# Optimization experiments

Measured on AMD Instinct MI355X. Metric: run time of the kernel, lower is better.

The kernel has to match this reference:

```python
import jax, jax.numpy as jnp
import numpy as np
import math

LMAX = 2
NUM_RBF = 32
CUTOFF = 5.0
MUL_EDGE = 4          # mul_per_l
N_NODES = 50000
N_EDGES = 800000
NODE_MULS = [64, 32, 16]   # multiplicities of 0e,1o,2e in node_irreps
MSG_MULS = [64, 32, 16]    # multiplicities of 0e,1o,2e in msg_irreps
NODE_DIM = sum(m * (2 * l + 1) for l, m in enumerate(NODE_MULS))  # 240
# parity-conserving CG paths (l1 from node, l2 from edge, l3 to msg)
PATHS = [(0,0,0),(1,1,0),(2,2,0),(0,1,1),(1,0,1),(1,2,1),(2,1,1),(0,2,2),(2,0,2),(1,1,2),(2,2,2)]
TP_SIZES = [NODE_MULS[l1]*MUL_EDGE*MSG_MULS[l3] for (l1,l2,l3) in PATHS]
FAN_IN = {l3: sum(NODE_MULS[p1]*MUL_EDGE for (p1,p2,p3) in PATHS if p3 == l3) for l3 in range(LMAX+1)}


def _su2_cg(j1, m1, j2, m2, j3, m3):
    # Racah formula for SU(2) Clebsch-Gordan coefficients (integer l)
    if m3 != m1 + m2:
        return 0.0
    f = lambda n: math.factorial(int(n))
    vmin = int(max(-j1 + j2 + m3, -j1 + m1, 0))
    vmax = int(min(j2 + j3 + m1, j3 - j1 + j2, j3 + m3))
    C = math.sqrt((2*j3+1) * f(j3+j1-j2) * f(j3-j1+j2) * f(j1+j2-j3) * f(j3+m3) * f(j3-m3)
                  / (f(j1+j2+j3+1) * f(j1-m1) * f(j1+m1) * f(j2-m2) * f(j2+m2)))
    S = 0.0
    for v in range(vmin, vmax+1):
        S += (-1.0)**(v + j2 + m2) * f(j2+j3+m1-v) * f(j1-m1+v) / (
            f(v) * f(j3-j1+j2-v) * f(j3+m3-v) * f(v+j1-j2-m3))
    return C * S


def _real_to_complex(l):
    # change of basis real spherical harmonics -> complex, with phase making 3j real
    q = np.zeros((2*l+1, 2*l+1), dtype=np.complex128)
    for m in range(-l, 0):
        q[l+m, l+abs(m)] = 1/math.sqrt(2)
        q[l+m, l-abs(m)] = -1j/math.sqrt(2)
    q[l, l] = 1.0
    for m in range(1, l+1):
        q[l+m, l+abs(m)] = (-1)**m / math.sqrt(2)
        q[l+m, l-abs(m)] = 1j*(-1)**m / math.sqrt(2)
    return (-1j)**l * q


def _wigner_3j(l1, l2, l3):
    C = np.zeros((2*l1+1, 2*l2+1, 2*l3+1))
    for m1 in range(-l1, l1+1):
        for m2 in range(-l2, l2+1):
            for m3 in range(-l3, l3+1):
                C[l1+m1, l2+m2, l3+m3] = _su2_cg(l1, m1, l2, m2, l3, m3)
    Q1, Q2, Q3 = _real_to_complex(l1), _real_to_complex(l2), _real_to_complex(l3)
    Cc = np.einsum('ij,kl,mn,ikn->jlm', Q1, Q2, np.conj(Q3).T, C.astype(np.complex128))
    Cr = np.real(Cc)
    if np.linalg.norm(Cr) < 1e-8:
        Cr = np.imag(Cc)
    return (Cr / np.linalg.norm(Cr)).astype(np.float32)

W3J = {p: jnp.asarray(_wigner_3j(*p)) for p in PATHS}


def setup_inputs() -> dict:
    key = jax.random.key(0)
    ks = jax.random.split(key, 8)
    node_feat = jax.random.normal(ks[0], (N_NODES, NODE_DIM), jnp.float32)
    edge_index = jax.random.randint(ks[1], (2, N_EDGES), 0, N_NODES)
    edge_vec = jax.random.normal(ks[2], (N_EDGES, 3), jnp.float32) * 1.5
    mask = jax.random.uniform(ks[3], (N_EDGES,), jnp.float32)
    mlp_w1 = jax.random.normal(ks[4], (LMAX+1, NUM_RBF, 32), jnp.float32) / math.sqrt(NUM_RBF)
    mlp_b1 = jnp.zeros((LMAX+1, 32), jnp.float32)
    mlp_w2 = jax.random.normal(ks[5], (LMAX+1, 32, MUL_EDGE), jnp.float32) / math.sqrt(32.0)
    mlp_b2 = jnp.zeros((LMAX+1, MUL_EDGE), jnp.float32)
    tp_w = jax.random.normal(ks[6], (sum(TP_SIZES),), jnp.float32)
    return {"node_feat": node_feat, "edge_index": edge_index, "edge_vec": edge_vec,
            "mask": mask, "mlp_w1": mlp_w1, "mlp_b1": mlp_b1,
            "mlp_w2": mlp_w2, "mlp_b2": mlp_b2, "tp_w": tp_w}


def reference(node_feat, edge_index, edge_vec, mask, mlp_w1, mlp_b1, mlp_w2, mlp_b2, tp_w):
    src = edge_index[0]
    r = jnp.maximum(jnp.linalg.norm(edge_vec, axis=-1, keepdims=True), 1e-12)   # [E,1]
    r_hat = edge_vec / r
    x, y, z = r_hat[:, 0], r_hat[:, 1], r_hat[:, 2]
    # --- RBFEmb (smooth cosine cutoff + gaussians in exp(-r) space), then the
    # extra rbounds factor applied again in _edge_features (faithful to source)
    rbounds = 0.5 * (jnp.cos(r * jnp.pi / CUTOFF) + 1.0)                         # [E,1]
    means = jnp.linspace(math.exp(-CUTOFF), 1.0, NUM_RBF).astype(edge_vec.dtype)
    beta = (2.0 / NUM_RBF * (1.0 - math.exp(-CUTOFF))) ** (-2)
    rbf = rbounds * (r < CUTOFF).astype(edge_vec.dtype) * jnp.exp(-beta * jnp.square(jnp.exp(-r) - means))
    rbf = rbounds * rbf                                                          # [E,NUM_RBF]
    # --- real spherical harmonics, e3nn 'component' normalization, l = 0,1,2
    s3, s5, s15 = math.sqrt(3.0), math.sqrt(5.0), math.sqrt(15.0)
    Y = [jnp.ones_like(x)[:, None],
         s3 * r_hat,
         jnp.stack([s15 * x * z, s15 * x * y, s5 * (y * y - 0.5 * (x * x + z * z)),
                    s15 * y * z, 0.5 * s15 * (z * z - x * x)], axis=-1)]
    # --- per-l radial MLP weights, outer product with Y_l -> edge irrep blocks
    edge_blocks = []
    for l in range(LMAX + 1):
        h = jax.nn.silu(rbf @ mlp_w1[l] + mlp_b1[l])
        w_l = h @ mlp_w2[l] + mlp_b2[l]                                          # [E,MUL_EDGE]
        edge_blocks.append(w_l[:, :, None] * Y[l][:, None, :])                   # [E,MUL_EDGE,2l+1]
    # --- gather node features per edge and split into irrep blocks
    f_i = node_feat[src]                                                         # [E,NODE_DIM]
    node_blocks, off = [], 0
    for l, mul in enumerate(NODE_MULS):
        d = mul * (2 * l + 1)
        node_blocks.append(f_i[:, off:off + d].reshape(-1, mul, 2 * l + 1))
        off += d
    # --- fully-connected CG tensor product (per-path small contractions)
    terms = {l3: [] for l3 in range(LMAX + 1)}
    woff = 0
    for (l1, l2, l3), sz in zip(PATHS, TP_SIZES):
        W = tp_w[woff:woff + sz].reshape(NODE_MULS[l1], MUL_EDGE, MSG_MULS[l3])
        woff += sz
        alpha = 1.0 / math.sqrt(FAN_IN[l3])
        terms[l3].append(alpha * jnp.einsum('eui,evj,uvw,ijk->ewk',
                                            node_blocks[l1], edge_blocks[l2], W,
                                            W3J[(l1, l2, l3)], optimize='optimal'))
    E = edge_vec.shape[0]
    msg_e = jnp.concatenate([sum(terms[l3]).reshape(E, -1) for l3 in range(LMAX + 1)], axis=-1)
    return msg_e * mask[:, None]
```

## Files before the change

### kernel.cpp

```cpp
#include <hip/hip_runtime.h>
#include <math.h>

#define TE 32
#define NODE_DIM 240
#define NPAD 248

typedef _Float16 f16;
typedef f16 f16x2 __attribute__((ext_vector_type(2)));
typedef f16 f16x4 __attribute__((ext_vector_type(4)));
typedef f16 f16x8 __attribute__((ext_vector_type(8)));
typedef float f32x4 __attribute__((ext_vector_type(4)));


struct cplx { double re, im; };
__device__ inline cplx cmul(cplx a, cplx b) {
    return { a.re*b.re - a.im*b.im, a.re*b.im + a.im*b.re };
}

__device__ double dfact(int n) { double r = 1.0; for (int i = 2; i <= n; ++i) r *= i; return r; }

__device__ double su2_cg(int j1, int m1, int j2, int m2, int j3, int m3) {
    if (m3 != m1 + m2) return 0.0;
    int vmin = max(max(-j1 + j2 + m3, -j1 + m1), 0);
    int vmax = min(min(j2 + j3 + m1, j3 - j1 + j2), j3 + m3);
    double C = sqrt((2.0*j3 + 1.0) * dfact(j3 + j1 - j2) * dfact(j3 - j1 + j2) * dfact(j1 + j2 - j3)
                    * dfact(j3 + m3) * dfact(j3 - m3)
                    / (dfact(j1 + j2 + j3 + 1) * dfact(j1 - m1) * dfact(j1 + m1)
                       * dfact(j2 - m2) * dfact(j2 + m2)));
    double S = 0.0;
    for (int v = vmin; v <= vmax; ++v) {
        double sgn = ((v + j2 + m2) & 1) ? -1.0 : 1.0;
        S += sgn * dfact(j2 + j3 + m1 - v) * dfact(j1 - m1 + v)
             / (dfact(v) * dfact(j3 - j1 + j2 - v) * dfact(j3 + m3 - v) * dfact(v + j1 - j2 - m3));
    }
    return C * S;
}

__device__ cplx rtc(int l, int a, int b) {
    double re = 0.0, im = 0.0;
    const double inv_s2 = 0.70710678118654752440;
    int m = a - l;
    if (m < 0) {
        if (b == l - m)      re = inv_s2;
        else if (b == l + m) im = -inv_s2;
    } else if (m == 0) {
        if (b == l) re = 1.0;
    } else {
        double s = (m & 1) ? -1.0 : 1.0;
        if (b == l + m)      re = s * inv_s2;
        else if (b == l - m) im = s * inv_s2;
    }
    if (l == 1) { double t = re; re = im; im = -t; }
    else if (l == 2) { re = -re; im = -im; }
    return { re, im };
}

__global__ void w3j_init(float* __restrict__ out) {
    __shared__ double sRe[363], sIm[363];
    __shared__ double sNorm[11];
    __shared__ int    sUse[11];
    const int L1A[11] = {0,1,2,0,1,1,2,0,2,1,2};
    const int L2A[11] = {0,1,2,1,0,2,1,2,0,1,2};
    const int L3A[11] = {0,0,0,1,1,1,1,2,2,2,2};
    const int OFF[12] = {0,1,10,35,44,53,98,143,168,193,238,363};
    int t = threadIdx.x;
    if (t < 363) {
        int p = 0;
        while (p < 10 && t >= OFF[p+1]) ++p;
        int rel = t - OFF[p];
        int a1 = L1A[p], a2 = L2A[p], a3 = L3A[p];
        int n1 = 2*a1 + 1, n2 = 2*a2 + 1, n3 = 2*a3 + 1;
        int jj = rel / (n2*n3), ll = (rel / n3) % n2, mm = rel % n3;
        double cr = 0.0, ci = 0.0;
        for (int i = 0; i < n1; ++i)
            for (int k = 0; k < n2; ++k)
                for (int n = 0; n < n3; ++n) {
                    double c = su2_cg(a1, i - a1, a2, k - a2, a3, n - a3);
                    if (c == 0.0) continue;
                    cplx q1 = rtc(a1, i, jj);
                    cplx q2 = rtc(a2, k, ll);
                    cplx q3 = rtc(a3, n, mm); q3.im = -q3.im;
                    cplx pr = cmul(cmul(q1, q2), q3);
                    cr += pr.re * c; ci += pr.im * c;
                }
        sRe[t] = cr; sIm[t] = ci;
    }
    __syncthreads();
    if (t < 11) {
        double nr = 0.0, ni = 0.0;
        for (int e = OFF[t]; e < OFF[t+1]; ++e) { nr += sRe[e]*sRe[e]; ni += sIm[e]*sIm[e]; }
        int use_im = (sqrt(nr) < 1e-8) ? 1 : 0;
        sUse[t] = use_im;
        sNorm[t] = sqrt(use_im ? ni : nr);
    }
    __syncthreads();
    if (t < 363) {
        int p = 0;
        while (p < 10 && t >= OFF[p+1]) ++p;
        out[t] = (float)((sUse[p] ? sIm[t] : sRe[t]) / sNorm[p]);
    }
}

__global__ void w_prep(const float* __restrict__ tp_w, f16* __restrict__ wpre) {
    const int WOFF[11] = {0,16384,24576,28672,36864,40960,45056,47104,51200,52224,54272};
    const int UA[11]   = {64,32,16,64,32,32,16,64,16,32,16};
    const int NA[11]   = {64,64,64,32,32,32,32,16,16,16,16};
    const int L3A[11]  = {0,0,0,1,1,1,1,2,2,2,2};
    const float alph[3] = { 1.0f/sqrtf(448.0f), 1.0f/24.0f, 1.0f/sqrtf(512.0f) };
    int tid = threadIdx.x;
    for (int p = 0; p < 11; ++p) {
        int U = UA[p], N = NA[p], woff = WOFF[p];
        int NT = N/16;
        int size = U*4*N;
        float alpha = alph[L3A[p]];
        for (int j = tid; j < size; j += 256) {
            int f = j >> 9, r = j & 511;
            int lane = r >> 3, jj = r & 7;
            int ks = f / NT, nt = f - ks*NT;
            int k = ks*32 + (lane>>4)*8 + jj;
            int n = nt*16 + (lane&15);
            wpre[woff + j] = (f16)(tp_w[woff + k*N + n] * alpha);
        }
    }
}

template<int l1, int l2, int l3>
__device__ __forceinline__ void path_mfma(
    int tid, int woff, int cgoff,
    const f16* __restrict__ wpre,
    const f16* sN16, const float (*sY)[8], const float* sW3,
    const f16x2 (*sWlPk)[6],
    f32x4 (&acc)[3])
{
    constexpr int U  = (l1 == 0) ? 64 : (l1 == 1) ? 32 : 16;
    constexpr int N  = (l3 == 0) ? 64 : (l3 == 1) ? 32 : 16;
    constexpr int NI = 2*l1 + 1, NJ = 2*l2 + 1, NK = 2*l3 + 1;
    constexpr int M  = NK * TE;
    constexpr int NODE_OFF = (l1 == 0) ? 0 : (l1 == 1) ? 64 : 160;
    constexpr int KS = U / 8;
    constexpr int NT = N / 16;
    constexpr int NTASKS = (M/16) * NT;

    const int wv = tid >> 6, lane = tid & 63;
    const int ln = tid & 15, qt = (tid & 63) >> 4;

    #pragma unroll
    for (int t = 0; t < 3; ++t) {
        int task = t*4 + wv;
        if (task < NTASKS) {
            int mt = task / NT, nt = task - mt*NT;
            int row = mt*16 + ln;
            int e = row & 31, kk = row >> 5;
            float cyr[NI];
            #pragma unroll
            for (int i = 0; i < NI; ++i) {
                float c = 0.f;
                #pragma unroll
                for (int j = 0; j < NJ; ++j) {
                    float yj = (l2 == 0) ? 1.f : ((l2 == 1) ? sY[e][j] : sY[e][3 + j]);
                    c += sW3[cgoff + (i*NJ + j)*NK + kk] * yj;
                }
                cyr[i] = c;
            }
            f16x2 wl0 = sWlPk[e][l2*2 + 0];
            f16x2 wl1 = sWlPk[e][l2*2 + 1];
            const f16* nbase = sN16 + e*NPAD + NODE_OFF;
            const f16* wbase = wpre + woff + (size_t)nt*512 + lane*8;
            #pragma unroll
            for (int ks = 0; ks < KS; ++ks) {
                f16x8 wf = *(const f16x8*)(wbase + (size_t)ks*NT*512);
                int u0 = ks*8 + qt*2;
                float b0 = 0.f, b1 = 0.f;
                #pragma unroll
                for (int i = 0; i < NI; ++i) {
                    b0 += (float)nbase[u0*NI + i]      * cyr[i];
                    b1 += (float)nbase[u0*NI + NI + i] * cyr[i];
                }
                f16 b0h = (f16)b0, b1h = (f16)b1;
                f16x2 bb0 = {b0h, b0h}, bb1 = {b1h, b1h};
                f16x2 a01 = bb0*wl0, a23 = bb0*wl1, a45 = bb1*wl0, a67 = bb1*wl1;
                f16x8 af = {a01[0],a01[1],a23[0],a23[1],a45[0],a45[1],a67[0],a67[1]};
                acc[t] = __builtin_amdgcn_mfma_f32_16x16x32_f16(af, wf, acc[t], 0, 0, 0);
            }
        }
    }
}

template<int NK, int NT, int NTASKS, int OFF>
__device__ __forceinline__ void store_group(int tid, const f32x4 (&acc)[3], f16* sAcc16)
{
    int wv = tid >> 6;
    int ln = tid & 15, qt = (tid & 63) >> 4;
    #pragma unroll
    for (int t = 0; t < 3; ++t) {
        int task = t*4 + wv;
        if (task < NTASKS) {
            int mt = task / NT, nt = task % NT;
            int kk = mt >> 1;
            int e0 = (mt & 1) * 16;
            #pragma unroll
            for (int r = 0; r < 4; ++r) {
                int e = e0 + qt*4 + r;
                sAcc16[e*240 + OFF + (nt*16 + ln)*NK + kk] = (f16)acc[t][r];
            }
        }
    }
}

__global__ __launch_bounds__(256, 4)
void edge_main(const float* __restrict__ node_feat,
               const int*   __restrict__ edge_src,
               const float* __restrict__ edge_vec,
               const float* __restrict__ maskp,
               const float* __restrict__ mlp_w1, const float* __restrict__ mlp_b1,
               const float* __restrict__ mlp_w2, const float* __restrict__ mlp_b2,
               const f16*   __restrict__ wpre,
               const float* __restrict__ w3j,
               float* __restrict__ out)
{
    __shared__ __align__(16) f16 sN16[TE*NPAD];
    __shared__ __align__(16) f16 sAcc16[TE*240];
    __shared__ float sW3[364];
    __shared__ float sY[TE][8];
    __shared__ f16x2 sWlPk[TE][6];

    float* sRbf  = (float*)sAcc16;
    float* sH    = sRbf + TE*32;
    float* sWl   = sH   + TE*32;
    float* sR    = sWl  + TE*12;
    float* sRb2  = sR   + TE;
    float* sMask = sRb2 + TE;
    int*   sSrc  = (int*)(sMask + TE);

    int tid = threadIdx.x;
    long eg0 = (long)blockIdx.x * TE;

    if (tid < TE) {
        long eg = eg0 + tid;
        float vx = edge_vec[eg*3 + 0], vy = edge_vec[eg*3 + 1], vz = edge_vec[eg*3 + 2];
        float rn = sqrtf(vx*vx + vy*vy + vz*vz);
        float r  = fmaxf(rn, 1e-12f);
        float inv = 1.0f / r;
        float x = vx*inv, y = vy*inv, z = vz*inv;
        sR[tid] = r;
        float rb = 0.5f * (cosf(r * 3.14159265358979323846f / 5.0f) + 1.0f);
        sRb2[tid] = (r < 5.0f) ? rb*rb : 0.0f;
        sMask[tid] = maskp[eg];
        sSrc[tid]  = edge_src[eg];
        const float s3 = sqrtf(3.0f), s5 = sqrtf(5.0f), s15 = sqrtf(15.0f);
        sY[tid][0] = s3*x; sY[tid][1] = s3*y; sY[tid][2] = s3*z;
        sY[tid][3] = s15*x*z;
        sY[tid][4] = s15*x*y;
        sY[tid][5] = s5*(y*y - 0.5f*(x*x + z*z));
        sY[tid][6] = s15*y*z;
        sY[tid][7] = 0.5f*s15*(z*z - x*x);
    }
    for (int t = tid; t < 363; t += 256) sW3[t] = w3j[t];
    __syncthreads();

    {
        float em5  = expf(-5.0f);
        float step = (1.0f - em5) / 31.0f;
        float beta = 256.0f / ((1.0f - em5) * (1.0f - em5));
        for (int idx = tid; idx < TE*32; idx += 256) {
            int e = idx >> 5, j = idx & 31;
            float mean = em5 + step * j;
            float d = expf(-sR[e]) - mean;
            sRbf[e*32 + j] = sRb2[e] * expf(-beta * d * d);
        }
    }
    for (int idx = tid; idx < TE*60; idx += 256) {
        int e = idx / 60, q = idx - e*60;
        f32x4 v = *(const f32x4*)(node_feat + (long)sSrc[e]*NODE_DIM + q*4);
        f16x4 h = {(f16)v.x, (f16)v.y, (f16)v.z, (f16)v.w};
        *(f16x4*)&sN16[e*NPAD + q*4] = h;
    }
    __syncthreads();

    for (int l = 0; l < 3; ++l) {
        for (int idx = tid; idx < TE*32; idx += 256) {
            int e = idx >> 5, j = idx & 31;
            float zacc = mlp_b1[l*32 + j];
            #pragma unroll 8
            for (int rr = 0; rr < 32; ++rr) zacc += sRbf[e*32 + rr] * mlp_w1[(l*32 + rr)*32 + j];
            sH[e*32 + j] = zacc / (1.0f + expf(-zacc));
        }
        __syncthreads();
        for (int idx = tid; idx < TE*4; idx += 256) {
            int e = idx >> 2, v = idx & 3;
            float zacc = mlp_b2[l*4 + v];
            #pragma unroll 8
            for (int j = 0; j < 32; ++j) zacc += sH[e*32 + j] * mlp_w2[(l*32 + j)*4 + v];
            sWl[e*12 + l*4 + v] = zacc;
        }
        __syncthreads();
    }
    for (int idx = tid; idx < TE*6; idx += 256) {
        int e = idx / 6, h = idx - e*6;
        int l = h >> 1, vh = h & 1;
        float m = sMask[e];
        f16x2 p = {(f16)(sWl[e*12 + l*4 + vh*2] * m), (f16)(sWl[e*12 + l*4 + vh*2 + 1] * m)};
        sWlPk[e][h] = p;
    }
    __syncthreads();

    f32x4 acc[3];

    #pragma unroll
    for (int t = 0; t < 3; ++t) acc[t] = {0.f, 0.f, 0.f, 0.f};
    path_mfma<0,0,0>(tid,     0,   0, wpre, sN16, sY, sW3, sWlPk, acc);
    path_mfma<1,1,0>(tid, 16384,   1, wpre, sN16, sY, sW3, sWlPk, acc);
    path_mfma<2,2,0>(tid, 24576,  10, wpre, sN16, sY, sW3, sWlPk, acc);
    store_group<1, 4, 8, 0>(tid, acc, sAcc16);

    #pragma unroll
    for (int t = 0; t < 3; ++t) acc[t] = {0.f, 0.f, 0.f, 0.f};
    path_mfma<0,1,1>(tid, 28672,  35, wpre, sN16, sY, sW3, sWlPk, acc);
    path_mfma<1,0,1>(tid, 36864,  44, wpre, sN16, sY, sW3, sWlPk, acc);
    path_mfma<1,2,1>(tid, 40960,  53, wpre, sN16, sY, sW3, sWlPk, acc);
    path_mfma<2,1,1>(tid, 45056,  98, wpre, sN16, sY, sW3, sWlPk, acc);
    store_group<3, 2, 12, 64>(tid, acc, sAcc16);

    #pragma unroll
    for (int t = 0; t < 3; ++t) acc[t] = {0.f, 0.f, 0.f, 0.f};
    path_mfma<0,2,2>(tid, 47104, 143, wpre, sN16, sY, sW3, sWlPk, acc);
    path_mfma<2,0,2>(tid, 51200, 168, wpre, sN16, sY, sW3, sWlPk, acc);
    path_mfma<1,1,2>(tid, 52224, 193, wpre, sN16, sY, sW3, sWlPk, acc);
    path_mfma<2,2,2>(tid, 54272, 238, wpre, sN16, sY, sW3, sWlPk, acc);
    store_group<5, 1, 10, 160>(tid, acc, sAcc16);

    __syncthreads();

    for (int idx = tid; idx < TE*30; idx += 256) {
        int e = idx / 30, q = idx - e*30;
        f16x8 v = *(const f16x8*)&sAcc16[e*240 + q*8];
        f32x4 lo = {(float)v[0], (float)v[1], (float)v[2], (float)v[3]};
        f32x4 hi = {(float)v[4], (float)v[5], (float)v[6], (float)v[7]};
        float* dst = out + (eg0 + e)*NODE_DIM + q*8;
        __builtin_nontemporal_store(lo, (f32x4*)dst);
        __builtin_nontemporal_store(hi, (f32x4*)(dst + 4));
    }
}

extern "C" void kernel_launch(void* const* d_in, const int* in_sizes, int n_in,
                              void* d_out, int out_size, void* d_ws, size_t ws_size,
                              hipStream_t stream)
{
    const float* node_feat = (const float*)d_in[0];
    const int*   edge_idx  = (const int*)  d_in[1];
    const float* edge_vec  = (const float*)d_in[2];
    const float* maskp     = (const float*)d_in[3];
    const float* mlp_w1    = (const float*)d_in[4];
    const float* mlp_b1    = (const float*)d_in[5];
    const float* mlp_w2    = (const float*)d_in[6];
    const float* mlp_b2    = (const float*)d_in[7];
    const float* tp_w      = (const float*)d_in[8];
    float* out  = (float*)d_out;
    float* w3j  = (float*)d_ws;
    f16*   wpre = (f16*)((char*)d_ws + 2048);

    int E = in_sizes[3];
    const int* edge_src = edge_idx;

    hipLaunchKernelGGL(w3j_init, dim3(1), dim3(512), 0, stream, w3j);
    hipLaunchKernelGGL(w_prep,   dim3(1), dim3(256), 0, stream, tp_w, wpre);
    hipLaunchKernelGGL(edge_main, dim3(E / TE), dim3(256), 0, stream,
                       node_feat, edge_src, edge_vec, maskp,
                       mlp_w1, mlp_b1, mlp_w2, mlp_b2, wpre, w3j, out);
}
```

Before: 1.173 ms.

## Pad node irrep blocks in LDS and use packed fdot2 for node-CG contraction

Node features are stored in shared memory with each l=1 and l=2 component group padded to 4 and 8 halfs, so one lane can fetch a multiplicity's components with a single 16-byte LDS load. The per-task CG-times-Y coefficients are precomputed once and packed to f16, and the node contraction uses packed fdot2 instead of scalar converts and FMAs. The loop order is also inverted so each weight fragment loaded from global memory is reused across all of a wave's M-tasks. In exchange, shared-memory use grows, the buffer must be zero-filled, the scatter into LDS for l>0 becomes scalar, and the coefficients lose precision by being rounded to f16.

```diff
diff --git a/kernel.cpp b/kernel.cpp
--- a/kernel.cpp
+++ b/kernel.cpp
@@ -3,13 +3,28 @@
 
 #define TE 32
 #define NODE_DIM 240
-#define NPAD 248
+#define ESTR 328
 
 typedef _Float16 f16;
 typedef f16 f16x2 __attribute__((ext_vector_type(2)));
 typedef f16 f16x4 __attribute__((ext_vector_type(4)));
 typedef f16 f16x8 __attribute__((ext_vector_type(8)));
 typedef float f32x4 __attribute__((ext_vector_type(4)));
+
+__device__ __forceinline__ float fdot2(f16x2 a, f16x2 b, float c) {
+#if __has_builtin(__builtin_amdgcn_fdot2)
+    return __builtin_amdgcn_fdot2(a, b, c, false);
+#else
+    return (float)a[0]*(float)b[0] + (float)a[1]*(float)b[1] + c;
+#endif
+}
+__device__ __forceinline__ f16x2 cvtpk(float a, float b) {
+#if __has_builtin(__builtin_amdgcn_cvt_pkrtz)
+    return __builtin_bit_cast(f16x2, __builtin_amdgcn_cvt_pkrtz(a, b));
+#else
+    f16x2 r = {(f16)a, (f16)b}; return r;
+#endif
+}
 
 
 struct cplx { double re, im; };
@@ -124,6 +139,12 @@
     }
 }
 
+__device__ __forceinline__ int node_slot(int ch) {
+    if (ch < 64) return ch;
+    if (ch < 160) { int t = ch - 64;  return 64  + (t/3)*4 + (t - (t/3)*3); }
+    { int t = ch - 160; return 192 + (t/5)*8 + (t - (t/5)*5); }
+}
+
 template<int l1, int l2, int l3>
 __device__ __forceinline__ void path_mfma(
     int tid, int woff, int cgoff,
@@ -136,21 +157,26 @@
     constexpr int N  = (l3 == 0) ? 64 : (l3 == 1) ? 32 : 16;
     constexpr int NI = 2*l1 + 1, NJ = 2*l2 + 1, NK = 2*l3 + 1;
     constexpr int M  = NK * TE;
-    constexpr int NODE_OFF = (l1 == 0) ? 0 : (l1 == 1) ? 64 : 160;
+    constexpr int SEC = (l1 == 0) ? 0 : (l1 == 1) ? 64 : 192;
     constexpr int KS = U / 8;
     constexpr int NT = N / 16;
     constexpr int NTASKS = (M/16) * NT;
+    constexpr int NW = (NTASKS + 3) / 4;
 
     const int wv = tid >> 6, lane = tid & 63;
     const int ln = tid & 15, qt = (tid & 63) >> 4;
-
-    #pragma unroll
-    for (int t = 0; t < 3; ++t) {
+    const int ntw = wv % NT;
+
+    const f16* nbT[NW];
+    f16x2 cyP[NW][3];
+    f16x2 wl0T[NW], wl1T[NW];
+    #pragma unroll
+    for (int t = 0; t < NW; ++t) {
         int task = t*4 + wv;
         if (task < NTASKS) {
-            int mt = task / NT, nt = task - mt*NT;
-            int row = mt*16 + ln;
-            int e = row & 31, kk = row >> 5;
+            int mt = task / NT;
+            int kk = mt >> 1;
+            int e  = (mt & 1)*16 + ln;
             float cyr[NI];
             #pragma unroll
             for (int i = 0; i < NI; ++i) {
@@ -162,23 +188,56 @@
                 }
                 cyr[i] = c;
             }
-            f16x2 wl0 = sWlPk[e][l2*2 + 0];
-            f16x2 wl1 = sWlPk[e][l2*2 + 1];
-            const f16* nbase = sN16 + e*NPAD + NODE_OFF;
-            const f16* wbase = wpre + woff + (size_t)nt*512 + lane*8;
-            #pragma unroll
-            for (int ks = 0; ks < KS; ++ks) {
-                f16x8 wf = *(const f16x8*)(wbase + (size_t)ks*NT*512);
-                int u0 = ks*8 + qt*2;
-                float b0 = 0.f, b1 = 0.f;
-                #pragma unroll
-                for (int i = 0; i < NI; ++i) {
-                    b0 += (float)nbase[u0*NI + i]      * cyr[i];
-                    b1 += (float)nbase[u0*NI + NI + i] * cyr[i];
+            if constexpr (NI == 1) {
+                cyP[t][0] = cvtpk(cyr[0], cyr[0]);
+            } else if constexpr (NI == 3) {
+                cyP[t][0] = cvtpk(cyr[0], cyr[1]);
+                cyP[t][1] = cvtpk(cyr[2], 0.f);
+            } else {
+                cyP[t][0] = cvtpk(cyr[0], cyr[1]);
+                cyP[t][1] = cvtpk(cyr[2], cyr[3]);
+                cyP[t][2] = cvtpk(cyr[4], 0.f);
+            }
+            wl0T[t] = sWlPk[e][l2*2 + 0];
+            wl1T[t] = sWlPk[e][l2*2 + 1];
+            nbT[t]  = sN16 + e*ESTR + SEC;
+        }
+    }
+
+    const f16* wbase = wpre + woff + (size_t)ntw*512 + lane*8;
+    #pragma unroll
+    for (int ks = 0; ks < KS; ++ks) {
+        f16x8 wf = *(const f16x8*)(wbase + (size_t)ks*NT*512);
+        const int u0 = ks*8 + qt*2;
+        #pragma unroll
+        for (int t = 0; t < NW; ++t) {
+            int task = t*4 + wv;
+            if (task < NTASKS) {
+                f16x2 bh;
+                if constexpr (NI == 1) {
+                    f16x2 n01 = *(const f16x2*)(nbT[t] + u0);
+                    bh = n01 * cyP[t][0];
+                } else if constexpr (NI == 3) {
+                    f16x8 n8 = *(const f16x8*)(nbT[t] + u0*4);
+                    float b0 = fdot2(f16x2{n8[0], n8[1]}, cyP[t][0], 0.f);
+                    b0 = fdot2(f16x2{n8[2], n8[3]}, cyP[t][1], b0);
+                    float b1 = fdot2(f16x2{n8[4], n8[5]}, cyP[t][0], 0.f);
+                    b1 = fdot2(f16x2{n8[6], n8[7]}, cyP[t][1], b1);
+                    bh = cvtpk(b0, b1);
+                } else {
+                    f16x8 na = *(const f16x8*)(nbT[t] + u0*8);
+                    f16x8 nb = *(const f16x8*)(nbT[t] + u0*8 + 8);
+                    float b0 = fdot2(f16x2{na[0], na[1]}, cyP[t][0], 0.f);
+                    b0 = fdot2(f16x2{na[2], na[3]}, cyP[t][1], b0);
+                    b0 = fdot2(f16x2{na[4], na[5]}, cyP[t][2], b0);
+                    float b1 = fdot2(f16x2{nb[0], nb[1]}, cyP[t][0], 0.f);
+                    b1 = fdot2(f16x2{nb[2], nb[3]}, cyP[t][1], b1);
+                    b1 = fdot2(f16x2{nb[4], nb[5]}, cyP[t][2], b1);
+                    bh = cvtpk(b0, b1);
                 }
-                f16 b0h = (f16)b0, b1h = (f16)b1;
-                f16x2 bb0 = {b0h, b0h}, bb1 = {b1h, b1h};
-                f16x2 a01 = bb0*wl0, a23 = bb0*wl1, a45 = bb1*wl0, a67 = bb1*wl1;
+                f16x2 b00 = {bh[0], bh[0]}, b11 = {bh[1], bh[1]};
+                f16x2 a01 = b00*wl0T[t], a23 = b00*wl1T[t];
+                f16x2 a45 = b11*wl0T[t], a67 = b11*wl1T[t];
                 f16x8 af = {a01[0],a01[1],a23[0],a23[1],a45[0],a45[1],a67[0],a67[1]};
                 acc[t] = __builtin_amdgcn_mfma_f32_16x16x32_f16(af, wf, acc[t], 0, 0, 0);
             }
@@ -218,7 +277,7 @@
                const float* __restrict__ w3j,
                float* __restrict__ out)
 {
-    __shared__ __align__(16) f16 sN16[TE*NPAD];
+    __shared__ __align__(16) f16 sN16[TE*ESTR];
     __shared__ __align__(16) f16 sAcc16[TE*240];
     __shared__ float sW3[364];
     __shared__ float sY[TE][8];
@@ -255,6 +314,10 @@
         sY[tid][6] = s15*y*z;
         sY[tid][7] = 0.5f*s15*(z*z - x*x);
     }
+    for (int idx = tid; idx < TE*(ESTR/8); idx += 256) {
+        f16x8 z = {0,0,0,0,0,0,0,0};
+        *(f16x8*)&sN16[idx*8] = z;
+    }
     for (int t = tid; t < 363; t += 256) sW3[t] = w3j[t];
     __syncthreads();
 
@@ -272,8 +335,16 @@
     for (int idx = tid; idx < TE*60; idx += 256) {
         int e = idx / 60, q = idx - e*60;
         f32x4 v = *(const f32x4*)(node_feat + (long)sSrc[e]*NODE_DIM + q*4);
-        f16x4 h = {(f16)v.x, (f16)v.y, (f16)v.z, (f16)v.w};
-        *(f16x4*)&sN16[e*NPAD + q*4] = h;
+        int ch = q*4;
+        if (ch < 64) {
+            f16x4 h = {(f16)v.x, (f16)v.y, (f16)v.z, (f16)v.w};
+            *(f16x4*)&sN16[e*ESTR + ch] = h;
+        } else {
+            sN16[e*ESTR + node_slot(ch+0)] = (f16)v.x;
+            sN16[e*ESTR + node_slot(ch+1)] = (f16)v.y;
+            sN16[e*ESTR + node_slot(ch+2)] = (f16)v.z;
+            sN16[e*ESTR + node_slot(ch+3)] = (f16)v.w;
+        }
     }
     __syncthreads();
 
```

Result: slower. 1.409 ms (+20.1%).

## Precompute CG-contracted node operands in LDS and store outputs directly

Applied to the files above, without the earlier changes.

For the l1>0 paths, the node-times-CG contraction B[e,k,u] is now built once per edge block into a shared LDS buffer, so it is no longer recomputed inside every MFMA task and K-step. The l1=0 paths get a separate routine that does the contraction with packed f16 multiplies. Each wave now keeps a fixed N-tile so its weight fragment load is reused across its M-tasks. Accumulators are written straight to global memory with scalar nontemporal stores, replacing the LDS staging and vectorized write-out. The cost is many extra __syncthreads barriers, uncoalesced scalar global stores, and more f16 rounding in the packed l0 path.

```diff
diff --git a/kernel.cpp b/kernel.cpp
--- a/kernel.cpp
+++ b/kernel.cpp
@@ -10,6 +10,14 @@
 typedef f16 f16x4 __attribute__((ext_vector_type(4)));
 typedef f16 f16x8 __attribute__((ext_vector_type(8)));
 typedef float f32x4 __attribute__((ext_vector_type(4)));
+
+__device__ __forceinline__ f16x2 cvtpk(float a, float b) {
+#if __has_builtin(__builtin_amdgcn_cvt_pkrtz)
+    return __builtin_bit_cast(f16x2, __builtin_amdgcn_cvt_pkrtz(a, b));
+#else
+    f16x2 r = {(f16)a, (f16)b}; return r;
+#endif
+}
 
 
 struct cplx { double re, im; };
@@ -125,60 +133,153 @@
 }
 
 template<int l1, int l2, int l3>
-__device__ __forceinline__ void path_mfma(
+__device__ __forceinline__ void build_B(
+    int tid, int cgoff, f16* B,
+    const f16* sN16, const float (*sY)[8], const float* sW3)
+{
+    constexpr int U  = (l1 == 1) ? 32 : 16;
+    constexpr int NI = 2*l1 + 1, NJ = 2*l2 + 1, NK = 2*l3 + 1;
+    constexpr int SEC = (l1 == 1) ? 64 : 160;
+    constexpr int UP = U + 2;
+
+    for (int idx = tid; idx < TE*NK; idx += 256) {
+        int e = idx / NK, kk = idx - e*NK;
+        float cyr[NI];
+        #pragma unroll
+        for (int i = 0; i < NI; ++i) {
+            float c = 0.f;
+            #pragma unroll
+            for (int j = 0; j < NJ; ++j) {
+                float yj = (l2 == 0) ? 1.f : ((l2 == 1) ? sY[e][j] : sY[e][3 + j]);
+                c += sW3[cgoff + (i*NJ + j)*NK + kk] * yj;
+            }
+            cyr[i] = c;
+        }
+        const f16* nb = sN16 + e*NPAD + SEC;
+        f16* brow = B + idx*UP;
+        #pragma unroll 4
+        for (int u = 0; u < U; ++u) {
+            float b = 0.f;
+            #pragma unroll
+            for (int i = 0; i < NI; ++i) b += (float)nb[u*NI + i] * cyr[i];
+            brow[u] = (f16)b;
+        }
+    }
+}
+
+template<int l1, int l2, int l3>
+__device__ __forceinline__ void mfma_B(
+    int tid, int woff,
+    const f16* __restrict__ wpre, const f16* B,
+    const f16x2 (*sWlPk)[6],
+    f32x4 (&acc)[3])
+{
+    constexpr int U  = (l1 == 1) ? 32 : 16;
+    constexpr int N  = (l3 == 0) ? 64 : (l3 == 1) ? 32 : 16;
+    constexpr int NK = 2*l3 + 1;
+    constexpr int M  = NK * TE;
+    constexpr int KS = U / 8;
+    constexpr int NT = N / 16;
+    constexpr int NTASKS = (M/16) * NT;
+    constexpr int NW = (NTASKS + 3) / 4;
+    constexpr int UP = U + 2;
+
+    const int wv = tid >> 6, lane = tid & 63;
+    const int ln = tid & 15, qt = (tid & 63) >> 4;
+    const int ntw = wv % NT;
+
+    const f16* browT[NW];
+    f16x2 wl0T[NW], wl1T[NW];
+    #pragma unroll
+    for (int t = 0; t < NW; ++t) {
+        int task = t*4 + wv;
+        if (task < NTASKS) {
+            int mt = task / NT;
+            int kk = mt >> 1;
+            int e  = (mt & 1)*16 + ln;
+            browT[t] = B + (e*NK + kk)*UP;
+            wl0T[t] = sWlPk[e][l2*2 + 0];
+            wl1T[t] = sWlPk[e][l2*2 + 1];
+        }
+    }
+
+    const f16* wbase = wpre + woff + (size_t)ntw*512 + lane*8;
+    #pragma unroll
+    for (int ks = 0; ks < KS; ++ks) {
+        f16x8 wf = *(const f16x8*)(wbase + (size_t)ks*NT*512);
+        const int u0 = ks*8 + qt*2;
+        #pragma unroll
+        for (int t = 0; t < NW; ++t) {
+            int task = t*4 + wv;
+            if (task < NTASKS) {
+                f16x2 bh = *(const f16x2*)(browT[t] + u0);
+                f16x2 b00 = {bh[0], bh[0]}, b11 = {bh[1], bh[1]};
+                f16x2 a01 = b00*wl0T[t], a23 = b00*wl1T[t];
+                f16x2 a45 = b11*wl0T[t], a67 = b11*wl1T[t];
+                f16x8 af = {a01[0],a01[1],a23[0],a23[1],a45[0],a45[1],a67[0],a67[1]};
+                acc[t] = __builtin_amdgcn_mfma_f32_16x16x32_f16(af, wf, acc[t], 0, 0, 0);
+            }
+        }
+    }
+}
+
+template<int l2, int l3>
+__device__ __forceinline__ void mfma_l0(
     int tid, int woff, int cgoff,
     const f16* __restrict__ wpre,
     const f16* sN16, const float (*sY)[8], const float* sW3,
     const f16x2 (*sWlPk)[6],
     f32x4 (&acc)[3])
 {
-    constexpr int U  = (l1 == 0) ? 64 : (l1 == 1) ? 32 : 16;
     constexpr int N  = (l3 == 0) ? 64 : (l3 == 1) ? 32 : 16;
-    constexpr int NI = 2*l1 + 1, NJ = 2*l2 + 1, NK = 2*l3 + 1;
+    constexpr int NJ = 2*l2 + 1, NK = 2*l3 + 1;
     constexpr int M  = NK * TE;
-    constexpr int NODE_OFF = (l1 == 0) ? 0 : (l1 == 1) ? 64 : 160;
-    constexpr int KS = U / 8;
+    constexpr int KS = 8;
     constexpr int NT = N / 16;
     constexpr int NTASKS = (M/16) * NT;
+    constexpr int NW = (NTASKS + 3) / 4;
 
     const int wv = tid >> 6, lane = tid & 63;
     const int ln = tid & 15, qt = (tid & 63) >> 4;
-
-    #pragma unroll
-    for (int t = 0; t < 3; ++t) {
+    const int ntw = wv % NT;
+
+    const f16* nbT[NW];
+    f16x2 cyP[NW];
+    f16x2 wl0T[NW], wl1T[NW];
+    #pragma unroll
+    for (int t = 0; t < NW; ++t) {
         int task = t*4 + wv;
         if (task < NTASKS) {
-            int mt = task / NT, nt = task - mt*NT;
-            int row = mt*16 + ln;
-            int e = row & 31, kk = row >> 5;
-            float cyr[NI];
+            int mt = task / NT;
+            int kk = mt >> 1;
+            int e  = (mt & 1)*16 + ln;
+            float c = 0.f;
             #pragma unroll
-            for (int i = 0; i < NI; ++i) {
-                float c = 0.f;
-                #pragma unroll
-                for (int j = 0; j < NJ; ++j) {
-                    float yj = (l2 == 0) ? 1.f : ((l2 == 1) ? sY[e][j] : sY[e][3 + j]);
-                    c += sW3[cgoff + (i*NJ + j)*NK + kk] * yj;
-                }
-                cyr[i] = c;
+            for (int j = 0; j < NJ; ++j) {
+                float yj = (l2 == 0) ? 1.f : ((l2 == 1) ? sY[e][j] : sY[e][3 + j]);
+                c += sW3[cgoff + j*NK + kk] * yj;
             }
-            f16x2 wl0 = sWlPk[e][l2*2 + 0];
-            f16x2 wl1 = sWlPk[e][l2*2 + 1];
-            const f16* nbase = sN16 + e*NPAD + NODE_OFF;
-            const f16* wbase = wpre + woff + (size_t)nt*512 + lane*8;
-            #pragma unroll
-            for (int ks = 0; ks < KS; ++ks) {
-                f16x8 wf = *(const f16x8*)(wbase + (size_t)ks*NT*512);
-                int u0 = ks*8 + qt*2;
-                float b0 = 0.f, b1 = 0.f;
-                #pragma unroll
-                for (int i = 0; i < NI; ++i) {
-                    b0 += (float)nbase[u0*NI + i]      * cyr[i];
-                    b1 += (float)nbase[u0*NI + NI + i] * cyr[i];
-                }
-                f16 b0h = (f16)b0, b1h = (f16)b1;
-                f16x2 bb0 = {b0h, b0h}, bb1 = {b1h, b1h};
-                f16x2 a01 = bb0*wl0, a23 = bb0*wl1, a45 = bb1*wl0, a67 = bb1*wl1;
+            cyP[t] = cvtpk(c, c);
+            wl0T[t] = sWlPk[e][l2*2 + 0];
+            wl1T[t] = sWlPk[e][l2*2 + 1];
+            nbT[t]  = sN16 + e*NPAD;
+        }
+    }
+
+    const f16* wbase = wpre + woff + (size_t)ntw*512 + lane*8;
+    #pragma unroll
+    for (int ks = 0; ks < KS; ++ks) {
+        f16x8 wf = *(const f16x8*)(wbase + (size_t)ks*NT*512);
+        const int u0 = ks*8 + qt*2;
+        #pragma unroll
+        for (int t = 0; t < NW; ++t) {
+            int task = t*4 + wv;
+            if (task < NTASKS) {
+                f16x2 n01 = *(const f16x2*)(nbT[t] + u0);
+                f16x2 bh = n01 * cyP[t];
+                f16x2 b00 = {bh[0], bh[0]}, b11 = {bh[1], bh[1]};
+                f16x2 a01 = b00*wl0T[t], a23 = b00*wl1T[t];
+                f16x2 a45 = b11*wl0T[t], a67 = b11*wl1T[t];
                 f16x8 af = {a01[0],a01[1],a23[0],a23[1],a45[0],a45[1],a67[0],a67[1]};
                 acc[t] = __builtin_amdgcn_mfma_f32_16x16x32_f16(af, wf, acc[t], 0, 0, 0);
             }
@@ -187,7 +288,8 @@
 }
 
 template<int NK, int NT, int NTASKS, int OFF>
-__device__ __forceinline__ void store_group(int tid, const f32x4 (&acc)[3], f16* sAcc16)
+__device__ __forceinline__ void store_direct(int tid, const f32x4 (&acc)[3],
+                                             float* __restrict__ out, long eg0)
 {
     int wv = tid >> 6;
     int ln = tid & 15, qt = (tid & 63) >> 4;
@@ -198,10 +300,11 @@
             int mt = task / NT, nt = task % NT;
             int kk = mt >> 1;
             int e0 = (mt & 1) * 16;
+            int ch = OFF + (nt*16 + ln)*NK + kk;
             #pragma unroll
             for (int r = 0; r < 4; ++r) {
                 int e = e0 + qt*4 + r;
-                sAcc16[e*240 + OFF + (nt*16 + ln)*NK + kk] = (f16)acc[t][r];
+                __builtin_nontemporal_store(acc[t][r], out + (eg0 + e)*NODE_DIM + ch);
             }
         }
     }
@@ -219,12 +322,12 @@
                float* __restrict__ out)
 {
     __shared__ __align__(16) f16 sN16[TE*NPAD];
-    __shared__ __align__(16) f16 sAcc16[TE*240];
+    __shared__ __align__(16) f16 Bls[8256];
     __shared__ float sW3[364];
     __shared__ float sY[TE][8];
     __shared__ f16x2 sWlPk[TE][6];
 
-    float* sRbf  = (float*)sAcc16;
+    float* sRbf  = (float*)Bls;
     float* sH    = sRbf + TE*32;
     float* sWl   = sH   + TE*32;
     float* sR    = sWl  + TE*12;
@@ -255,6 +358,10 @@
         sY[tid][6] = s15*y*z;
         sY[tid][7] = 0.5f*s15*(z*z - x*x);
     }
+    for (int idx = tid; idx < TE*(NPAD/8); idx += 256) {
+        f16x8 z = {0,0,0,0,0,0,0,0};
+        *(f16x8*)&sN16[idx*8] = z;
+    }
     for (int t = tid; t < 363; t += 256) sW3[t] = w3j[t];
     __syncthreads();
 
@@ -306,40 +413,45 @@
 
     f32x4 acc[3];
 
+    build_B<1,1,0>(tid,   1, Bls,        sN16, sY, sW3);
+    build_B<2,2,0>(tid,  10, Bls + 1088, sN16, sY, sW3);
+    __syncthreads();
     #pragma unroll
     for (int t = 0; t < 3; ++t) acc[t] = {0.f, 0.f, 0.f, 0.f};
-    path_mfma<0,0,0>(tid,     0,   0, wpre, sN16, sY, sW3, sWlPk, acc);
-    path_mfma<1,1,0>(tid, 16384,   1, wpre, sN16, sY, sW3, sWlPk, acc);
-    path_mfma<2,2,0>(tid, 24576,  10, wpre, sN16, sY, sW3, sWlPk, acc);
-    store_group<1, 4, 8, 0>(tid, acc, sAcc16);
-
+    mfma_l0<0,0>(tid,     0,   0, wpre, sN16, sY, sW3, sWlPk, acc);
+    mfma_B<1,1,0>(tid, 16384, wpre, Bls,        sWlPk, acc);
+    mfma_B<2,2,0>(tid, 24576, wpre, Bls + 1088, sWlPk, acc);
+    store_direct<1, 4, 8, 0>(tid, acc, out, eg0);
+    __syncthreads();
+
+    build_B<1,0,1>(tid,  44, Bls,        sN16, sY, sW3);
+    build_B<1,2,1>(tid,  53, Bls + 3264, sN16, sY, sW3);
+    build_B<2,1,1>(tid,  98, Bls + 6528, sN16, sY, sW3);
+    __syncthreads();
     #pragma unroll
     for (int t = 0; t < 3; ++t) acc[t] = {0.f, 0.f, 0.f, 0.f};
-    path_mfma<0,1,1>(tid, 28672,  35, wpre, sN16, sY, sW3, sWlPk, acc);
-    path_mfma<1,0,1>(tid, 36864,  44, wpre, sN16, sY, sW3, sWlPk, acc);
-    path_mfma<1,2,1>(tid, 40960,  53, wpre, sN16, sY, sW3, sWlPk, acc);
-    path_mfma<2,1,1>(tid, 45056,  98, wpre, sN16, sY, sW3, sWlPk, acc);
-    store_group<3, 2, 12, 64>(tid, acc, sAcc16);
+    mfma_l0<1,1>(tid, 28672,  35, wpre, sN16, sY, sW3, sWlPk, acc);
+    mfma_B<1,0,1>(tid, 36864, wpre, Bls,        sWlPk, acc);
+    mfma_B<1,2,1>(tid, 40960, wpre, Bls + 3264, sWlPk, acc);
+    mfma_B<2,1,1>(tid, 45056, wpre, Bls + 6528, sWlPk, acc);
+    store_direct<3, 2, 12, 64>(tid, acc, out, eg0);
 
     #pragma unroll
     for (int t = 0; t < 3; ++t) acc[t] = {0.f, 0.f, 0.f, 0.f};
-    path_mfma<0,2,2>(tid, 47104, 143, wpre, sN16, sY, sW3, sWlPk, acc);
-    path_mfma<2,0,2>(tid, 51200, 168, wpre, sN16, sY, sW3, sWlPk, acc);
-    path_mfma<1,1,2>(tid, 52224, 193, wpre, sN16, sY, sW3, sWlPk, acc);
-    path_mfma<2,2,2>(tid, 54272, 238, wpre, sN16, sY, sW3, sWlPk, acc);
-    store_group<5, 1, 10, 160>(tid, acc, sAcc16);
-
-    __syncthreads();
-
-    for (int idx = tid; idx < TE*30; idx += 256) {
-        int e = idx / 30, q = idx - e*30;
-        f16x8 v = *(const f16x8*)&sAcc16[e*240 + q*8];
-        f32x4 lo = {(float)v[0], (float)v[1], (float)v[2], (float)v[3]};
-        f32x4 hi = {(float)v[4], (float)v[5], (float)v[6], (float)v[7]};
-        float* dst = out + (eg0 + e)*NODE_DIM + q*8;
-        __builtin_nontemporal_store(lo, (f32x4*)dst);
-        __builtin_nontemporal_store(hi, (f32x4*)(dst + 4));
-    }
+    mfma_l0<2,2>(tid, 47104, 143, wpre, sN16, sY, sW3, sWlPk, acc);
+    __syncthreads();
+    build_B<2,0,2>(tid, 168, Bls, sN16, sY, sW3);
+    __syncthreads();
+    mfma_B<2,0,2>(tid, 51200, wpre, Bls, sWlPk, acc);
+    __syncthreads();
+    build_B<1,1,2>(tid, 193, Bls, sN16, sY, sW3);
+    __syncthreads();
+    mfma_B<1,1,2>(tid, 52224, wpre, Bls, sWlPk, acc);
+    __syncthreads();
+    build_B<2,2,2>(tid, 238, Bls, sN16, sY, sW3);
+    __syncthreads();
+    mfma_B<2,2,2>(tid, 54272, wpre, Bls, sWlPk, acc);
+    store_direct<5, 1, 10, 160>(tid, acc, out, eg0);
 }
 
 extern "C" void kernel_launch(void* const* d_in, const int* in_sizes, int n_in,
```

New measurement: 1.481 ms. +26.3%, slower.

## Specialize l1=0 paths: MFMA raw node features, apply edge weights afterward

Applied to the files above, without the earlier changes.

For the three CG paths with scalar node input (l1=0), the MFMA now multiplies the raw 64-wide node scalars directly by weights laid out per edge-multiplicity v. The per-edge radial weight and the Y/CG factor are applied to the fp32 results after the MFMA, instead of being folded into the A operand per k-step. The weight prep reorders these paths to a v-grouped layout. The generic path also hoists its per-task CG coefficients and pointers out of the k loop, so each weight fragment is loaded once and reused across tasks. This removes the per-element scalar A construction for the largest path. In exchange it issues more MFMAs, four v slices with zero-initialized accumulators, and raises register pressure. A cvtpk helper is added but never used.

```diff
diff --git a/kernel.cpp b/kernel.cpp
--- a/kernel.cpp
+++ b/kernel.cpp
@@ -10,6 +10,14 @@
 typedef f16 f16x4 __attribute__((ext_vector_type(4)));
 typedef f16 f16x8 __attribute__((ext_vector_type(8)));
 typedef float f32x4 __attribute__((ext_vector_type(4)));
+
+__device__ __forceinline__ f16x2 cvtpk(float a, float b) {
+#if __has_builtin(__builtin_amdgcn_cvt_pkrtz)
+    return __builtin_bit_cast(f16x2, __builtin_amdgcn_cvt_pkrtz(a, b));
+#else
+    f16x2 r = {(f16)a, (f16)b}; return r;
+#endif
+}
 
 
 struct cplx { double re, im; };
@@ -106,6 +114,7 @@
     const int UA[11]   = {64,32,16,64,32,32,16,64,16,32,16};
     const int NA[11]   = {64,64,64,32,32,32,32,16,16,16,16};
     const int L3A[11]  = {0,0,0,1,1,1,1,2,2,2,2};
+    const int VG[11]   = {1,0,0,1,0,0,0,1,0,0,0};
     const float alph[3] = { 1.0f/sqrtf(448.0f), 1.0f/24.0f, 1.0f/sqrtf(512.0f) };
     int tid = threadIdx.x;
     for (int p = 0; p < 11; ++p) {
@@ -116,10 +125,102 @@
         for (int j = tid; j < size; j += 256) {
             int f = j >> 9, r = j & 511;
             int lane = r >> 3, jj = r & 7;
-            int ks = f / NT, nt = f - ks*NT;
-            int k = ks*32 + (lane>>4)*8 + jj;
-            int n = nt*16 + (lane&15);
+            int k, n;
+            if (VG[p]) {
+                int nt = f % NT; int tmp = f / NT;
+                int ks = tmp & 1; int v = tmp >> 1;
+                int u = ks*32 + (lane>>4)*8 + jj;
+                k = u*4 + v;
+                n = nt*16 + (lane&15);
+            } else {
+                int ks = f / NT, nt = f - ks*NT;
+                k = ks*32 + (lane>>4)*8 + jj;
+                n = nt*16 + (lane&15);
+            }
             wpre[woff + j] = (f16)(tp_w[woff + k*N + n] * alpha);
+        }
+    }
+}
+
+template<int l2, int l3>
+__device__ __forceinline__ void mfma_l0v(
+    int tid, int woff, int cgoff,
+    const f16* __restrict__ wpre,
+    const f16* sN16, const float (*sY)[8], const float* sW3,
+    const f16x2 (*sWlPk)[6],
+    f32x4 (&acc)[3])
+{
+    constexpr int N  = (l3 == 0) ? 64 : (l3 == 1) ? 32 : 16;
+    constexpr int NK = 2*l3 + 1;
+    constexpr int M  = NK * TE;
+    constexpr int NT = N / 16;
+    constexpr int NTASKS = (M/16) * NT;
+    constexpr int NW = (NTASKS + 3) / 4;
+
+    const int wv = tid >> 6, lane = tid & 63;
+    const int ln = tid & 15, qt = (tid & 63) >> 4;
+    const int ntw = wv % NT;
+
+    f16x8 af[NW][2];
+    int e0T[NW], kkT[NW];
+    #pragma unroll
+    for (int t = 0; t < NW; ++t) {
+        int task = t*4 + wv;
+        if (task < NTASKS) {
+            int mt = task / NT;
+            kkT[t] = mt >> 1;
+            e0T[t] = (mt & 1) * 16;
+            const f16* nb = sN16 + (e0T[t] + ln)*NPAD;
+            af[t][0] = *(const f16x8*)(nb + qt*8);
+            af[t][1] = *(const f16x8*)(nb + 32 + qt*8);
+        }
+    }
+
+    const f16* wbase = wpre + woff + (size_t)ntw*512 + lane*8;
+    #pragma unroll
+    for (int vh = 0; vh < 2; ++vh) {
+        f32x4 Q[NW][2];
+        #pragma unroll
+        for (int vv = 0; vv < 2; ++vv) {
+            const int v = vh*2 + vv;
+            f16x8 wf0 = *(const f16x8*)(wbase + (size_t)((v*2 + 0)*NT)*512);
+            f16x8 wf1 = *(const f16x8*)(wbase + (size_t)((v*2 + 1)*NT)*512);
+            #pragma unroll
+            for (int t = 0; t < NW; ++t) {
+                int task = t*4 + wv;
+                if (task < NTASKS) {
+                    f32x4 z = {0.f, 0.f, 0.f, 0.f};
+                    Q[t][vv] = __builtin_amdgcn_mfma_f32_16x16x32_f16(af[t][0], wf0, z, 0, 0, 0);
+                    Q[t][vv] = __builtin_amdgcn_mfma_f32_16x16x32_f16(af[t][1], wf1, Q[t][vv], 0, 0, 0);
+                }
+            }
+        }
+        #pragma unroll
+        for (int t = 0; t < NW; ++t) {
+            int task = t*4 + wv;
+            if (task < NTASKS) {
+                int kk = kkT[t];
+                #pragma unroll
+                for (int r = 0; r < 4; ++r) {
+                    int e = e0T[t] + qt*4 + r;
+                    f16x2 wlp = sWlPk[e][l2*2 + vh];
+                    float cy;
+                    if constexpr (l2 == 0) {
+                        cy = sW3[cgoff];
+                    } else if constexpr (l2 == 1) {
+                        cy = sW3[cgoff + 0*NK + kk]*sY[e][0]
+                           + sW3[cgoff + 1*NK + kk]*sY[e][1]
+                           + sW3[cgoff + 2*NK + kk]*sY[e][2];
+                    } else {
+                        cy = 0.f;
+                        #pragma unroll
+                        for (int j = 0; j < 5; ++j)
+                            cy += sW3[cgoff + j*NK + kk]*sY[e][3 + j];
+                    }
+                    float s = (float)wlp[0]*Q[t][0][r] + (float)wlp[1]*Q[t][1][r];
+                    acc[t][r] += cy * s;
+                }
+            }
         }
     }
 }
@@ -136,22 +237,26 @@
     constexpr int N  = (l3 == 0) ? 64 : (l3 == 1) ? 32 : 16;
     constexpr int NI = 2*l1 + 1, NJ = 2*l2 + 1, NK = 2*l3 + 1;
     constexpr int M  = NK * TE;
-    constexpr int NODE_OFF = (l1 == 0) ? 0 : (l1 == 1) ? 64 : 160;
+    constexpr int SEC = (l1 == 0) ? 0 : (l1 == 1) ? 64 : 160;
     constexpr int KS = U / 8;
     constexpr int NT = N / 16;
     constexpr int NTASKS = (M/16) * NT;
+    constexpr int NW = (NTASKS + 3) / 4;
 
     const int wv = tid >> 6, lane = tid & 63;
     const int ln = tid & 15, qt = (tid & 63) >> 4;
-
-    #pragma unroll
-    for (int t = 0; t < 3; ++t) {
+    const int ntw = wv % NT;
+
+    const f16* nbT[NW];
+    float cyT[NW][NI];
+    f16x2 wl0T[NW], wl1T[NW];
+    #pragma unroll
+    for (int t = 0; t < NW; ++t) {
         int task = t*4 + wv;
         if (task < NTASKS) {
-            int mt = task / NT, nt = task - mt*NT;
-            int row = mt*16 + ln;
-            int e = row & 31, kk = row >> 5;
-            float cyr[NI];
+            int mt = task / NT;
+            int kk = mt >> 1;
+            int e  = (mt & 1)*16 + ln;
             #pragma unroll
             for (int i = 0; i < NI; ++i) {
                 float c = 0.f;
@@ -160,27 +265,35 @@
                     float yj = (l2 == 0) ? 1.f : ((l2 == 1) ? sY[e][j] : sY[e][3 + j]);
                     c += sW3[cgoff + (i*NJ + j)*NK + kk] * yj;
                 }
-                cyr[i] = c;
-            }
-            f16x2 wl0 = sWlPk[e][l2*2 + 0];
-            f16x2 wl1 = sWlPk[e][l2*2 + 1];
-            const f16* nbase = sN16 + e*NPAD + NODE_OFF;
-            const f16* wbase = wpre + woff + (size_t)nt*512 + lane*8;
-            #pragma unroll
-            for (int ks = 0; ks < KS; ++ks) {
-                f16x8 wf = *(const f16x8*)(wbase + (size_t)ks*NT*512);
-                int u0 = ks*8 + qt*2;
+                cyT[t][i] = c;
+            }
+            wl0T[t] = sWlPk[e][l2*2 + 0];
+            wl1T[t] = sWlPk[e][l2*2 + 1];
+            nbT[t]  = sN16 + e*NPAD + SEC;
+        }
+    }
+
+    const f16* wbase = wpre + woff + (size_t)ntw*512 + lane*8;
+    #pragma unroll
+    for (int ks = 0; ks < KS; ++ks) {
+        f16x8 wf = *(const f16x8*)(wbase + (size_t)ks*NT*512);
+        const int u0 = ks*8 + qt*2;
+        #pragma unroll
+        for (int t = 0; t < NW; ++t) {
+            int task = t*4 + wv;
+            if (task < NTASKS) {
                 float b0 = 0.f, b1 = 0.f;
                 #pragma unroll
                 for (int i = 0; i < NI; ++i) {
-                    b0 += (float)nbase[u0*NI + i]      * cyr[i];
-                    b1 += (float)nbase[u0*NI + NI + i] * cyr[i];
+                    b0 += (float)nbT[t][u0*NI + i]      * cyT[t][i];
+                    b1 += (float)nbT[t][u0*NI + NI + i] * cyT[t][i];
                 }
                 f16 b0h = (f16)b0, b1h = (f16)b1;
-                f16x2 bb0 = {b0h, b0h}, bb1 = {b1h, b1h};
-                f16x2 a01 = bb0*wl0, a23 = bb0*wl1, a45 = bb1*wl0, a67 = bb1*wl1;
-                f16x8 af = {a01[0],a01[1],a23[0],a23[1],a45[0],a45[1],a67[0],a67[1]};
-                acc[t] = __builtin_amdgcn_mfma_f32_16x16x32_f16(af, wf, acc[t], 0, 0, 0);
+                f16x2 b00 = {b0h, b0h}, b11 = {b1h, b1h};
+                f16x2 a01 = b00*wl0T[t], a23 = b00*wl1T[t];
+                f16x2 a45 = b11*wl0T[t], a67 = b11*wl1T[t];
+                f16x8 afv = {a01[0],a01[1],a23[0],a23[1],a45[0],a45[1],a67[0],a67[1]};
+                acc[t] = __builtin_amdgcn_mfma_f32_16x16x32_f16(afv, wf, acc[t], 0, 0, 0);
             }
         }
     }
@@ -308,14 +421,14 @@
 
     #pragma unroll
     for (int t = 0; t < 3; ++t) acc[t] = {0.f, 0.f, 0.f, 0.f};
-    path_mfma<0,0,0>(tid,     0,   0, wpre, sN16, sY, sW3, sWlPk, acc);
+    mfma_l0v<0,0>(tid,     0,   0, wpre, sN16, sY, sW3, sWlPk, acc);
     path_mfma<1,1,0>(tid, 16384,   1, wpre, sN16, sY, sW3, sWlPk, acc);
     path_mfma<2,2,0>(tid, 24576,  10, wpre, sN16, sY, sW3, sWlPk, acc);
     store_group<1, 4, 8, 0>(tid, acc, sAcc16);
 
     #pragma unroll
     for (int t = 0; t < 3; ++t) acc[t] = {0.f, 0.f, 0.f, 0.f};
-    path_mfma<0,1,1>(tid, 28672,  35, wpre, sN16, sY, sW3, sWlPk, acc);
+    mfma_l0v<1,1>(tid, 28672,  35, wpre, sN16, sY, sW3, sWlPk, acc);
     path_mfma<1,0,1>(tid, 36864,  44, wpre, sN16, sY, sW3, sWlPk, acc);
     path_mfma<1,2,1>(tid, 40960,  53, wpre, sN16, sY, sW3, sWlPk, acc);
     path_mfma<2,1,1>(tid, 45056,  98, wpre, sN16, sY, sW3, sWlPk, acc);
@@ -323,7 +436,7 @@
 
     #pragma unroll
     for (int t = 0; t < 3; ++t) acc[t] = {0.f, 0.f, 0.f, 0.f};
-    path_mfma<0,2,2>(tid, 47104, 143, wpre, sN16, sY, sW3, sWlPk, acc);
+    mfma_l0v<2,2>(tid, 47104, 143, wpre, sN16, sY, sW3, sWlPk, acc);
     path_mfma<2,0,2>(tid, 51200, 168, wpre, sN16, sY, sW3, sWlPk, acc);
     path_mfma<1,1,2>(tid, 52224, 193, wpre, sN16, sY, sW3, sWlPk, acc);
     path_mfma<2,2,2>(tid, 54272, 238, wpre, sN16, sY, sW3, sWlPk, acc);
```

Result: slower. 1.552 ms (+32.3%).
